# Performance work log

Hardware: AMD Instinct MI355X
Metric: run time of the kernel (lower is better)

Reference implementation:

```python
import jax, jax.numpy as jnp
import numpy as np

EPS = 1e-5
N_LAYERS_TOTAL = 4  # n_layers + 1 convs


def setup_inputs() -> dict:
    key = jax.random.key(0)
    ks = jax.random.split(key, 6)
    B, N, C = 16, 2048, 128
    x = jax.random.normal(ks[0], (B, N, C), dtype=jnp.float32)
    adj = jax.random.uniform(ks[1], (B, N, N), dtype=jnp.float32)
    # per-layer params: weight [L,Cin,Cout], bias [L,Cout], bn gamma/beta [L,C]
    W = jax.random.normal(ks[2], (N_LAYERS_TOTAL, C, C), dtype=jnp.float32) * (1.0 / np.sqrt(C))
    b = jnp.zeros((N_LAYERS_TOTAL, C), dtype=jnp.float32)
    gamma = jnp.ones((N_LAYERS_TOTAL, C), dtype=jnp.float32)
    beta = jnp.zeros((N_LAYERS_TOTAL, C), dtype=jnp.float32)
    return {"x": x, "adj": adj, "W": W, "b": b, "gamma": gamma, "beta": beta}


def reference(x, adj, W, b, gamma, beta):
    # Stacked dense GCNConv -> ReLU -> BatchNorm1d (training mode).
    h = x
    for i in range(N_LAYERS_TOTAL):
        # GCNConv (dense, normalize=False): adj @ (h @ W) + b
        h = jnp.einsum('bnm,bmc->bnc', adj, h @ W[i]) + b[i]  # [B,N,C]
        h = jax.nn.relu(h)
        # BatchNorm over flattened (B*N) per channel, biased variance
        mu = jnp.mean(h, axis=(0, 1))
        var = jnp.mean(jnp.square(h - mu), axis=(0, 1))
        h = gamma[i] * (h - mu) * jax.lax.rsqrt(var + EPS) + beta[i]
    return h
```

## Files before the change

### kernel.cpp

```cpp
#include <hip/hip_runtime.h>
#include <stdint.h>
#include <stddef.h>

#define BATCH 16
#define NROW 2048
#define CH 128
#define NLAYER 4
#define NN_TOT (BATCH * NROW)
#define EPSV 1e-5f
#define KS 64

typedef short short8 __attribute__((ext_vector_type(8)));
typedef float f32x4 __attribute__((ext_vector_type(4)));

static __device__ __forceinline__ unsigned short f2bf(float f) {
  union { float f; unsigned int i; } v;
  v.f = f;
  unsigned int u = v.i;
  return (unsigned short)((u + 0x7FFFu + ((u >> 16) & 1u)) >> 16);
}

__global__ void init_kernel(const float* __restrict__ W,
                            unsigned short* __restrict__ Wt4,
                            float* __restrict__ gsum, float* __restrict__ gsumsq) {
  const int l = blockIdx.x;
  const int t = threadIdx.x;
  if (l < NLAYER) {
    const float* Wl = W + (size_t)l * CH * CH;
    unsigned short* Wo = Wt4 + (size_t)l * CH * CH;
    for (int idx = t; idx < CH * CH; idx += 256) {
      int o = idx >> 7, c = idx & 127;
      Wo[idx] = f2bf(Wl[c * CH + o]);
    }
  } else {
    for (int i = t; i < NLAYER * CH; i += 256) { gsum[i] = 0.0f; gsumsq[i] = 0.0f; }
  }
}

template <int FIRST>
__global__ __launch_bounds__(256) void gemm1_kernel(
    const float* __restrict__ X,
    const unsigned short* __restrict__ Wt,
    const float* __restrict__ gp, const float* __restrict__ bp,
    const float* __restrict__ gsumP, const float* __restrict__ gsumsqP,
    unsigned short* __restrict__ Yt) {
  __shared__ unsigned short As[64 * 128];
  __shared__ unsigned short Bs[128 * 128];
  __shared__ __align__(16) float ss[CH];
  __shared__ __align__(16) float tt[CH];
  const int tid = threadIdx.x;
  const int m0 = blockIdx.x * 64;

  if (!FIRST) {
    if (tid < CH) {
      const float inv = 1.0f / (float)NN_TOT;
      float mu = gsumP[tid] * inv;
      float var = gsumsqP[tid] * inv - mu * mu;
      float s_ = gp[tid] * rsqrtf(var + EPSV);
      ss[tid] = s_;
      tt[tid] = bp[tid] - mu * s_;
    }
    __syncthreads();
  }

#pragma unroll
  for (int j = 0; j < 4; ++j) {
    int c = tid + 256 * j;
    int r = c >> 4, slot = c & 15;
    int kc = slot ^ (r & 15);
    const float* p = X + (size_t)(m0 + r) * CH + kc * 8;
    f32x4 a = *(const f32x4*)p;
    f32x4 b = *(const f32x4*)(p + 4);
    if (!FIRST) {
      f32x4 sa = *(const f32x4*)(ss + kc * 8);
      f32x4 sb = *(const f32x4*)(ss + kc * 8 + 4);
      f32x4 ta = *(const f32x4*)(tt + kc * 8);
      f32x4 tb = *(const f32x4*)(tt + kc * 8 + 4);
      a = sa * a + ta;
      b = sb * b + tb;
    }
    short8 v;
    v[0] = (short)f2bf(a[0]); v[1] = (short)f2bf(a[1]);
    v[2] = (short)f2bf(a[2]); v[3] = (short)f2bf(a[3]);
    v[4] = (short)f2bf(b[0]); v[5] = (short)f2bf(b[1]);
    v[6] = (short)f2bf(b[2]); v[7] = (short)f2bf(b[3]);
    *(short8*)(As + c * 8) = v;
  }
#pragma unroll
  for (int j = 0; j < 8; ++j) {
    int c = tid + 256 * j;
    int r = c >> 4, slot = c & 15;
    int kc = slot ^ (r & 15);
    *(short8*)(Bs + c * 8) = *(const short8*)(Wt + (size_t)r * CH + kc * 8);
  }
  __syncthreads();

  const int l = tid & 63, w = tid >> 6;
  const int mq = (w >> 1) * 32, oq = (w & 1) * 64;
  const int lr = l & 15, lq = l >> 4;
  f32x4 acc[2][4] = {};

#pragma unroll
  for (int kt = 0; kt < 4; ++kt) {
    const int kc0 = kt * 4 + lq;
    const int slotK = kc0 ^ lr;
    short8 a[2], b[4];
#pragma unroll
    for (int mi = 0; mi < 2; ++mi)
      a[mi] = *(const short8*)(As + (mq + mi * 16 + lr) * 128 + slotK * 8);
#pragma unroll
    for (int ni = 0; ni < 4; ++ni)
      b[ni] = *(const short8*)(Bs + (oq + ni * 16 + lr) * 128 + slotK * 8);
#pragma unroll
    for (int mi = 0; mi < 2; ++mi)
#pragma unroll
      for (int ni = 0; ni < 4; ++ni)
        acc[mi][ni] = __builtin_amdgcn_mfma_f32_16x16x32_bf16(a[mi], b[ni], acc[mi][ni], 0, 0, 0);
  }

  const int bat = m0 >> 11;
  const int mb = m0 & 2047;
  unsigned short* YtB = Yt + (size_t)bat * CH * NROW;
#pragma unroll
  for (int ni = 0; ni < 4; ++ni) {
    const int o = oq + ni * 16 + lr;
    unsigned short* row = YtB + (size_t)o * NROW;
#pragma unroll
    for (int mi = 0; mi < 2; ++mi) {
      const int m = mb + mq + mi * 16 + lq * 4;
      f32x4 v = acc[mi][ni];
      unsigned short p0 = f2bf(v[0]), p1 = f2bf(v[1]);
      unsigned short p2 = f2bf(v[2]), p3 = f2bf(v[3]);
      unsigned long long packed = (unsigned long long)p0 | ((unsigned long long)p1 << 16) |
                                  ((unsigned long long)p2 << 32) | ((unsigned long long)p3 << 48);
      *(unsigned long long*)(row + m) = packed;
    }
  }
}

struct Pf {
  short8 a0, a1, a2, a3;
  short8 b0, b1;
  f32x4 f0, f1, f2, f3;
};

template <int CVT>
__global__ __launch_bounds__(256) void gemm2_kernel(
    const float* __restrict__ adjF,
    const unsigned short* __restrict__ adjH,
    unsigned short* __restrict__ adjO,
    const unsigned short* __restrict__ Yt,
    const float* __restrict__ bias,
    float* __restrict__ R,
    float* __restrict__ gsumL, float* __restrict__ gsumsqL) {
  __shared__ unsigned short As[2][CH * KS];
  __shared__ unsigned short Bs[2][64 * KS];
  __shared__ float redS[2][CH];
  __shared__ float redQ[2][CH];

  const int tid = threadIdx.x;
  const int bat = blockIdx.x >> 5;
  const int n0 = (blockIdx.x & 31) * 64;
  const unsigned short* YtB = Yt + (size_t)bat * CH * NROW;

  const int s8 = tid & 7;
  const int r8 = tid >> 3;
  const int swz8 = (s8 ^ (r8 & 7)) * 8;

  const unsigned short* gA0 = YtB + (size_t)r8 * NROW + s8 * 8;
  const unsigned short* gA1 = gA0 + (size_t)32 * NROW;
  const unsigned short* gA2 = gA0 + (size_t)64 * NROW;
  const unsigned short* gA3 = gA0 + (size_t)96 * NROW;
  const int lA0 = r8 * KS + swz8;
  const int lA1 = lA0 + 32 * KS;
  const int lA2 = lA0 + 64 * KS;
  const int lA3 = lA0 + 96 * KS;

  const size_t bO0 = (size_t)bat * NROW * NROW + (size_t)(n0 + r8) * NROW + s8 * 8;
  const size_t bO1 = bO0 + (size_t)32 * NROW;
  const int lB0 = r8 * KS + swz8;
  const int lB1 = lB0 + 32 * KS;

  const int l = tid & 63, w = tid >> 6;
  const int cq = (w >> 1) * 64;
  const int nh = (w & 1) * 32;
  const int lr = l & 15, lq = l >> 4;
  const int rsw = lr & 7;

  f32x4 acc[4][2] = {};

  auto LOADS = [&](Pf& p, int kt) {
    const int k0 = kt * KS;
    p.a0 = *(const short8*)(gA0 + k0);
    p.a1 = *(const short8*)(gA1 + k0);
    p.a2 = *(const short8*)(gA2 + k0);
    p.a3 = *(const short8*)(gA3 + k0);
    if constexpr (CVT) {
      const float* q0 = adjF + bO0 + k0;
      const float* q1 = adjF + bO1 + k0;
      p.f0 = *(const f32x4*)q0; p.f1 = *(const f32x4*)(q0 + 4);
      p.f2 = *(const f32x4*)q1; p.f3 = *(const f32x4*)(q1 + 4);
    } else {
      p.b0 = *(const short8*)(adjH + bO0 + k0);
      p.b1 = *(const short8*)(adjH + bO1 + k0);
    }
  };

  auto WRITES = [&](Pf& p, int buf, int kt) {
    unsigned short* Ap = As[buf];
    *(short8*)(Ap + lA0) = p.a0;
    *(short8*)(Ap + lA1) = p.a1;
    *(short8*)(Ap + lA2) = p.a2;
    *(short8*)(Ap + lA3) = p.a3;
    unsigned short* Bp = Bs[buf];
    if constexpr (CVT) {
      short8 q0, q1;
      q0[0] = (short)f2bf(p.f0[0]); q0[1] = (short)f2bf(p.f0[1]);
      q0[2] = (short)f2bf(p.f0[2]); q0[3] = (short)f2bf(p.f0[3]);
      q0[4] = (short)f2bf(p.f1[0]); q0[5] = (short)f2bf(p.f1[1]);
      q0[6] = (short)f2bf(p.f1[2]); q0[7] = (short)f2bf(p.f1[3]);
      q1[0] = (short)f2bf(p.f2[0]); q1[1] = (short)f2bf(p.f2[1]);
      q1[2] = (short)f2bf(p.f2[2]); q1[3] = (short)f2bf(p.f2[3]);
      q1[4] = (short)f2bf(p.f3[0]); q1[5] = (short)f2bf(p.f3[1]);
      q1[6] = (short)f2bf(p.f3[2]); q1[7] = (short)f2bf(p.f3[3]);
      *(short8*)(Bp + lB0) = q0;
      *(short8*)(Bp + lB1) = q1;
      const int k0 = kt * KS;
      *(short8*)(adjO + bO0 + k0) = q0;
      *(short8*)(adjO + bO1 + k0) = q1;
    } else {
      *(short8*)(Bp + lB0) = p.b0;
      *(short8*)(Bp + lB1) = p.b1;
    }
  };

  auto COMPUTE = [&](int buf) {
    const unsigned short* Ap = As[buf];
    const unsigned short* Bp = Bs[buf];
#pragma unroll
    for (int ks = 0; ks < 2; ++ks) {
      const int sl = ((ks * 4 + lq) ^ rsw) * 8;
      short8 a0 = *(const short8*)(Ap + (cq +  0 + lr) * KS + sl);
      short8 a1 = *(const short8*)(Ap + (cq + 16 + lr) * KS + sl);
      short8 a2 = *(const short8*)(Ap + (cq + 32 + lr) * KS + sl);
      short8 a3 = *(const short8*)(Ap + (cq + 48 + lr) * KS + sl);
      short8 b0 = *(const short8*)(Bp + (nh +  0 + lr) * KS + sl);
      short8 b1 = *(const short8*)(Bp + (nh + 16 + lr) * KS + sl);
      acc[0][0] = __builtin_amdgcn_mfma_f32_16x16x32_bf16(a0, b0, acc[0][0], 0, 0, 0);
      acc[0][1] = __builtin_amdgcn_mfma_f32_16x16x32_bf16(a0, b1, acc[0][1], 0, 0, 0);
      acc[1][0] = __builtin_amdgcn_mfma_f32_16x16x32_bf16(a1, b0, acc[1][0], 0, 0, 0);
      acc[1][1] = __builtin_amdgcn_mfma_f32_16x16x32_bf16(a1, b1, acc[1][1], 0, 0, 0);
      acc[2][0] = __builtin_amdgcn_mfma_f32_16x16x32_bf16(a2, b0, acc[2][0], 0, 0, 0);
      acc[2][1] = __builtin_amdgcn_mfma_f32_16x16x32_bf16(a2, b1, acc[2][1], 0, 0, 0);
      acc[3][0] = __builtin_amdgcn_mfma_f32_16x16x32_bf16(a3, b0, acc[3][0], 0, 0, 0);
      acc[3][1] = __builtin_amdgcn_mfma_f32_16x16x32_bf16(a3, b1, acc[3][1], 0, 0, 0);
    }
  };

#define BAR() do { asm volatile("s_waitcnt lgkmcnt(0)"); __builtin_amdgcn_s_barrier(); } while (0)

  Pf s0, s1;
  LOADS(s0, 0);
  WRITES(s0, 0, 0);
  LOADS(s0, 1);
  LOADS(s1, 2);
  BAR();

#pragma unroll 1
  for (int kt2 = 0; kt2 < 14; ++kt2) {
    const int kt = kt2 * 2;
    COMPUTE(0);
    WRITES(s0, 1, kt + 1);
    LOADS(s0, kt + 3);
    BAR();
    COMPUTE(1);
    WRITES(s1, 0, kt + 2);
    LOADS(s1, kt + 4);
    BAR();
  }
  COMPUTE(0);
  WRITES(s0, 1, 29);
  LOADS(s0, 31);
  BAR();
  COMPUTE(1);
  WRITES(s1, 0, 30);
  BAR();
  COMPUTE(0);
  WRITES(s0, 1, 31);
  BAR();
  COMPUTE(1);
#undef BAR

  float* RB = R + (size_t)bat * NROW * CH;
  f32x4 sumv[4] = {};
  f32x4 sumq[4] = {};
#pragma unroll
  for (int mi = 0; mi < 4; ++mi) {
    const int c0 = cq + mi * 16 + lq * 4;
    f32x4 bia = *(const f32x4*)(bias + c0);
#pragma unroll
    for (int ni = 0; ni < 2; ++ni) {
      const int n = n0 + nh + ni * 16 + lr;
      f32x4 v = acc[mi][ni] + bia;
      v[0] = fmaxf(v[0], 0.0f);
      v[1] = fmaxf(v[1], 0.0f);
      v[2] = fmaxf(v[2], 0.0f);
      v[3] = fmaxf(v[3], 0.0f);
      sumv[mi] += v;
      sumq[mi] += v * v;
      *(f32x4*)(RB + (size_t)n * CH + c0) = v;
    }
  }
#pragma unroll
  for (int mi = 0; mi < 4; ++mi) {
#pragma unroll
    for (int d = 1; d < 16; d <<= 1) {
      sumv[mi][0] += __shfl_xor(sumv[mi][0], d);
      sumv[mi][1] += __shfl_xor(sumv[mi][1], d);
      sumv[mi][2] += __shfl_xor(sumv[mi][2], d);
      sumv[mi][3] += __shfl_xor(sumv[mi][3], d);
      sumq[mi][0] += __shfl_xor(sumq[mi][0], d);
      sumq[mi][1] += __shfl_xor(sumq[mi][1], d);
      sumq[mi][2] += __shfl_xor(sumq[mi][2], d);
      sumq[mi][3] += __shfl_xor(sumq[mi][3], d);
    }
  }
  const int nqi = w & 1;
  if (lr == 0) {
#pragma unroll
    for (int mi = 0; mi < 4; ++mi) {
      const int c0 = cq + mi * 16 + lq * 4;
      redS[nqi][c0 + 0] = sumv[mi][0];
      redS[nqi][c0 + 1] = sumv[mi][1];
      redS[nqi][c0 + 2] = sumv[mi][2];
      redS[nqi][c0 + 3] = sumv[mi][3];
      redQ[nqi][c0 + 0] = sumq[mi][0];
      redQ[nqi][c0 + 1] = sumq[mi][1];
      redQ[nqi][c0 + 2] = sumq[mi][2];
      redQ[nqi][c0 + 3] = sumq[mi][3];
    }
  }
  __syncthreads();
  if (tid < CH) {
    atomicAdd(gsumL + tid, redS[0][tid] + redS[1][tid]);
  } else {
    const int c = tid - CH;
    atomicAdd(gsumsqL + c, redQ[0][c] + redQ[1][c]);
  }
}

__global__ __launch_bounds__(256) void out_kernel(
    float* __restrict__ out,
    const float* __restrict__ g3, const float* __restrict__ b3,
    const float* __restrict__ gsum3, const float* __restrict__ gsumsq3) {
  __shared__ __align__(16) float ss[CH];
  __shared__ __align__(16) float tt[CH];
  if (threadIdx.x < CH) {
    const float inv = 1.0f / (float)NN_TOT;
    float mu = gsum3[threadIdx.x] * inv;
    float var = gsumsq3[threadIdx.x] * inv - mu * mu;
    float s_ = g3[threadIdx.x] * rsqrtf(var + EPSV);
    ss[threadIdx.x] = s_;
    tt[threadIdx.x] = b3[threadIdx.x] - mu * s_;
  }
  __syncthreads();
  const int total = NN_TOT * CH / 4;
  for (int idx = blockIdx.x * blockDim.x + threadIdx.x; idx < total;
       idx += gridDim.x * blockDim.x) {
    f32x4 v = *(f32x4*)(out + (size_t)idx * 4);
    const int c0 = (idx & 31) * 4;
    f32x4 s = *(const f32x4*)(ss + c0);
    f32x4 t = *(const f32x4*)(tt + c0);
    v = s * v + t;
    *(f32x4*)(out + (size_t)idx * 4) = v;
  }
}

extern "C" void kernel_launch(void* const* d_in, const int* in_sizes, int n_in,
                              void* d_out, int out_size, void* d_ws, size_t ws_size,
                              hipStream_t stream) {
  (void)in_sizes; (void)n_in; (void)out_size; (void)ws_size;
  const float* x     = (const float*)d_in[0];
  const float* adj   = (const float*)d_in[1];
  const float* W     = (const float*)d_in[2];
  const float* bvec  = (const float*)d_in[3];
  const float* gamma = (const float*)d_in[4];
  const float* beta  = (const float*)d_in[5];

  float* R = (float*)d_out;

  char* ws = (char*)d_ws;
  unsigned short* adjb = (unsigned short*)(ws);
  unsigned short* Yt   = (unsigned short*)(ws + 134217728);
  unsigned short* Wt4  = (unsigned short*)(ws + 142606336);
  float* gsum   = (float*)(ws + 142606336 + 131072);
  float* gsumsq = (float*)(ws + 142606336 + 131072 + 2048);

  init_kernel<<<NLAYER + 1, 256, 0, stream>>>(W, Wt4, gsum, gsumsq);

  for (int i = 0; i < NLAYER; ++i) {
    if (i == 0) {
      gemm1_kernel<1><<<512, 256, 0, stream>>>(
          x, Wt4, nullptr, nullptr, nullptr, nullptr, Yt);
      gemm2_kernel<1><<<512, 256, 0, stream>>>(
          adj, nullptr, adjb, Yt, bvec, R, gsum, gsumsq);
    } else {
      gemm1_kernel<0><<<512, 256, 0, stream>>>(
          R, Wt4 + (size_t)i * CH * CH,
          gamma + (size_t)(i - 1) * CH, beta + (size_t)(i - 1) * CH,
          gsum + (size_t)(i - 1) * CH, gsumsq + (size_t)(i - 1) * CH, Yt);
      gemm2_kernel<0><<<512, 256, 0, stream>>>(
          nullptr, adjb, nullptr, Yt, bvec + (size_t)i * CH, R,
          gsum + (size_t)i * CH, gsumsq + (size_t)i * CH);
    }
  }
  out_kernel<<<512, 256, 0, stream>>>(R, gamma + 3 * CH, beta + 3 * CH,
                                      gsum + 3 * CH, gsumsq + 3 * CH);
}
```

Before: 587.9 us.

## Fuse all layer kernels into one persistent kernel with software grid barriers

Replaces the nine per-layer GEMM and output launches with a single persistent kernel of 256 blocks. Each block processes two tiles per phase, and a global atomic-counter barrier separates the phases. Shared memory is overlaid through a union across phases. The aim is to remove kernel launch gaps and tail effects between layers. In exchange it halves the grid, so each block does serial work, and it adds spin-barrier latency. The barrier also assumes all 256 blocks are co-resident, and it has a timeout fallback that could break correctness.

```diff
diff --git a/kernel.cpp b/kernel.cpp
--- a/kernel.cpp
+++ b/kernel.cpp
@@ -9,6 +9,8 @@
 #define NN_TOT (BATCH * NROW)
 #define EPSV 1e-5f
 #define KS 64
+#define GRID_P 256
+#define NTILE 512
 
 typedef short short8 __attribute__((ext_vector_type(8)));
 typedef float f32x4 __attribute__((ext_vector_type(4)));
@@ -20,9 +22,34 @@
   return (unsigned short)((u + 0x7FFFu + ((u >> 16) & 1u)) >> 16);
 }
 
+union __align__(16) SM {
+  struct { unsigned short As[64 * 128];
+           unsigned short Bs[128 * 128];
+           float ss[CH]; float tt[CH]; } g1;
+  struct { unsigned short As[2][CH * KS];
+           unsigned short Bs[2][64 * KS];
+           float redS[2][CH]; float redQ[2][CH]; } g2;
+  struct { float ss[CH]; float tt[CH]; } o;
+};
+
+static __device__ __forceinline__ void grid_sync(unsigned* cnt, unsigned target) {
+  __syncthreads();
+  if (threadIdx.x == 0) {
+    __hip_atomic_fetch_add(cnt, 1u, __ATOMIC_RELEASE, __HIP_MEMORY_SCOPE_AGENT);
+    unsigned long long t0 = __builtin_amdgcn_s_memrealtime();
+    while (__hip_atomic_load(cnt, __ATOMIC_RELAXED, __HIP_MEMORY_SCOPE_AGENT) < target) {
+      __builtin_amdgcn_s_sleep(8);
+      if (__builtin_amdgcn_s_memrealtime() - t0 > 200000000ull) break;
+    }
+    (void)__hip_atomic_load(cnt, __ATOMIC_ACQUIRE, __HIP_MEMORY_SCOPE_AGENT);
+  }
+  __syncthreads();
+}
+
 __global__ void init_kernel(const float* __restrict__ W,
                             unsigned short* __restrict__ Wt4,
-                            float* __restrict__ gsum, float* __restrict__ gsumsq) {
+                            float* __restrict__ gsum, float* __restrict__ gsumsq,
+                            unsigned* __restrict__ bar) {
   const int l = blockIdx.x;
   const int t = threadIdx.x;
   if (l < NLAYER) {
@@ -34,24 +61,24 @@
     }
   } else {
     for (int i = t; i < NLAYER * CH; i += 256) { gsum[i] = 0.0f; gsumsq[i] = 0.0f; }
-  }
-}
-
-template <int FIRST>
-__global__ __launch_bounds__(256) void gemm1_kernel(
-    const float* __restrict__ X,
-    const unsigned short* __restrict__ Wt,
+    if (t == 0) *bar = 0u;
+  }
+}
+
+static __device__ void gemm1_phase(
+    SM& sm, const float* __restrict__ X, const unsigned short* __restrict__ Wt,
     const float* __restrict__ gp, const float* __restrict__ bp,
     const float* __restrict__ gsumP, const float* __restrict__ gsumsqP,
-    unsigned short* __restrict__ Yt) {
-  __shared__ unsigned short As[64 * 128];
-  __shared__ unsigned short Bs[128 * 128];
-  __shared__ __align__(16) float ss[CH];
-  __shared__ __align__(16) float tt[CH];
-  const int tid = threadIdx.x;
-  const int m0 = blockIdx.x * 64;
-
-  if (!FIRST) {
+    unsigned short* __restrict__ Yt, const int first, const int tile, const int tid) {
+  unsigned short* As = sm.g1.As;
+  unsigned short* Bs = sm.g1.Bs;
+  float* ss = sm.g1.ss;
+  float* tt = sm.g1.tt;
+  const int m0 = tile * 64;
+
+  __syncthreads();
+
+  if (!first) {
     if (tid < CH) {
       const float inv = 1.0f / (float)NN_TOT;
       float mu = gsumP[tid] * inv;
@@ -71,7 +98,7 @@
     const float* p = X + (size_t)(m0 + r) * CH + kc * 8;
     f32x4 a = *(const f32x4*)p;
     f32x4 b = *(const f32x4*)(p + 4);
-    if (!FIRST) {
+    if (!first) {
       f32x4 sa = *(const f32x4*)(ss + kc * 8);
       f32x4 sb = *(const f32x4*)(ss + kc * 8 + 4);
       f32x4 ta = *(const f32x4*)(tt + kc * 8);
@@ -145,22 +172,15 @@
 };
 
 template <int CVT>
-__global__ __launch_bounds__(256) void gemm2_kernel(
-    const float* __restrict__ adjF,
-    const unsigned short* __restrict__ adjH,
-    unsigned short* __restrict__ adjO,
-    const unsigned short* __restrict__ Yt,
-    const float* __restrict__ bias,
-    float* __restrict__ R,
-    float* __restrict__ gsumL, float* __restrict__ gsumsqL) {
-  __shared__ unsigned short As[2][CH * KS];
-  __shared__ unsigned short Bs[2][64 * KS];
-  __shared__ float redS[2][CH];
-  __shared__ float redQ[2][CH];
-
-  const int tid = threadIdx.x;
-  const int bat = blockIdx.x >> 5;
-  const int n0 = (blockIdx.x & 31) * 64;
+static __device__ void gemm2_phase(
+    SM& sm,
+    const float* __restrict__ adjF, const unsigned short* __restrict__ adjH,
+    unsigned short* __restrict__ adjO, const unsigned short* __restrict__ Yt,
+    const float* __restrict__ bias, float* __restrict__ R,
+    float* __restrict__ gsumL, float* __restrict__ gsumsqL,
+    const int tile, const int tid) {
+  const int bat = tile >> 5;
+  const int n0 = (tile & 31) * 64;
   const unsigned short* YtB = Yt + (size_t)bat * CH * NROW;
 
   const int s8 = tid & 7;
@@ -207,12 +227,12 @@
   };
 
   auto WRITES = [&](Pf& p, int buf, int kt) {
-    unsigned short* Ap = As[buf];
+    unsigned short* Ap = sm.g2.As[buf];
     *(short8*)(Ap + lA0) = p.a0;
     *(short8*)(Ap + lA1) = p.a1;
     *(short8*)(Ap + lA2) = p.a2;
     *(short8*)(Ap + lA3) = p.a3;
-    unsigned short* Bp = Bs[buf];
+    unsigned short* Bp = sm.g2.Bs[buf];
     if constexpr (CVT) {
       short8 q0, q1;
       q0[0] = (short)f2bf(p.f0[0]); q0[1] = (short)f2bf(p.f0[1]);
@@ -235,8 +255,8 @@
   };
 
   auto COMPUTE = [&](int buf) {
-    const unsigned short* Ap = As[buf];
-    const unsigned short* Bp = Bs[buf];
+    const unsigned short* Ap = sm.g2.As[buf];
+    const unsigned short* Bp = sm.g2.Bs[buf];
 #pragma unroll
     for (int ks = 0; ks < 2; ++ks) {
       const int sl = ((ks * 4 + lq) ^ rsw) * 8;
@@ -261,6 +281,7 @@
 
   Pf s0, s1;
   LOADS(s0, 0);
+  __syncthreads();
   WRITES(s0, 0, 0);
   LOADS(s0, 1);
   LOADS(s1, 2);
@@ -326,47 +347,49 @@
     }
   }
   const int nqi = w & 1;
+  __syncthreads();
   if (lr == 0) {
 #pragma unroll
     for (int mi = 0; mi < 4; ++mi) {
       const int c0 = cq + mi * 16 + lq * 4;
-      redS[nqi][c0 + 0] = sumv[mi][0];
-      redS[nqi][c0 + 1] = sumv[mi][1];
-      redS[nqi][c0 + 2] = sumv[mi][2];
-      redS[nqi][c0 + 3] = sumv[mi][3];
-      redQ[nqi][c0 + 0] = sumq[mi][0];
-      redQ[nqi][c0 + 1] = sumq[mi][1];
-      redQ[nqi][c0 + 2] = sumq[mi][2];
-      redQ[nqi][c0 + 3] = sumq[mi][3];
+      sm.g2.redS[nqi][c0 + 0] = sumv[mi][0];
+      sm.g2.redS[nqi][c0 + 1] = sumv[mi][1];
+      sm.g2.redS[nqi][c0 + 2] = sumv[mi][2];
+      sm.g2.redS[nqi][c0 + 3] = sumv[mi][3];
+      sm.g2.redQ[nqi][c0 + 0] = sumq[mi][0];
+      sm.g2.redQ[nqi][c0 + 1] = sumq[mi][1];
+      sm.g2.redQ[nqi][c0 + 2] = sumq[mi][2];
+      sm.g2.redQ[nqi][c0 + 3] = sumq[mi][3];
     }
   }
   __syncthreads();
   if (tid < CH) {
-    atomicAdd(gsumL + tid, redS[0][tid] + redS[1][tid]);
+    atomicAdd(gsumL + tid, sm.g2.redS[0][tid] + sm.g2.redS[1][tid]);
   } else {
     const int c = tid - CH;
-    atomicAdd(gsumsqL + c, redQ[0][c] + redQ[1][c]);
-  }
-}
-
-__global__ __launch_bounds__(256) void out_kernel(
-    float* __restrict__ out,
+    atomicAdd(gsumsqL + c, sm.g2.redQ[0][c] + sm.g2.redQ[1][c]);
+  }
+}
+
+static __device__ void out_phase(
+    SM& sm, float* __restrict__ out,
     const float* __restrict__ g3, const float* __restrict__ b3,
-    const float* __restrict__ gsum3, const float* __restrict__ gsumsq3) {
-  __shared__ __align__(16) float ss[CH];
-  __shared__ __align__(16) float tt[CH];
-  if (threadIdx.x < CH) {
+    const float* __restrict__ gsum3, const float* __restrict__ gsumsq3,
+    const int blk, const int tid) {
+  float* ss = sm.o.ss;
+  float* tt = sm.o.tt;
+  __syncthreads();
+  if (tid < CH) {
     const float inv = 1.0f / (float)NN_TOT;
-    float mu = gsum3[threadIdx.x] * inv;
-    float var = gsumsq3[threadIdx.x] * inv - mu * mu;
-    float s_ = g3[threadIdx.x] * rsqrtf(var + EPSV);
-    ss[threadIdx.x] = s_;
-    tt[threadIdx.x] = b3[threadIdx.x] - mu * s_;
+    float mu = gsum3[tid] * inv;
+    float var = gsumsq3[tid] * inv - mu * mu;
+    float s_ = g3[tid] * rsqrtf(var + EPSV);
+    ss[tid] = s_;
+    tt[tid] = b3[tid] - mu * s_;
   }
   __syncthreads();
   const int total = NN_TOT * CH / 4;
-  for (int idx = blockIdx.x * blockDim.x + threadIdx.x; idx < total;
-       idx += gridDim.x * blockDim.x) {
+  for (int idx = blk * 256 + tid; idx < total; idx += GRID_P * 256) {
     f32x4 v = *(f32x4*)(out + (size_t)idx * 4);
     const int c0 = (idx & 31) * 4;
     f32x4 s = *(const f32x4*)(ss + c0);
@@ -374,6 +397,45 @@
     v = s * v + t;
     *(f32x4*)(out + (size_t)idx * 4) = v;
   }
+}
+
+__global__ __launch_bounds__(256, 2) void fused_kernel(
+    const float* __restrict__ x, const float* __restrict__ adj,
+    const float* __restrict__ W, const float* __restrict__ bvec,
+    const float* __restrict__ gamma, const float* __restrict__ beta,
+    float* __restrict__ R, unsigned short* __restrict__ adjb,
+    unsigned short* __restrict__ Yt, unsigned short* __restrict__ Wt4,
+    float* __restrict__ gsum, float* __restrict__ gsumsq,
+    unsigned* __restrict__ bar) {
+  __shared__ SM sm;
+  const int blk = blockIdx.x, tid = threadIdx.x;
+  unsigned tgt = 0;
+
+  gemm1_phase(sm, x, Wt4, nullptr, nullptr, nullptr, nullptr, Yt, 1, blk, tid);
+  gemm1_phase(sm, x, Wt4, nullptr, nullptr, nullptr, nullptr, Yt, 1, blk + GRID_P, tid);
+  tgt += GRID_P; grid_sync(bar, tgt);
+  gemm2_phase<1>(sm, adj, nullptr, adjb, Yt, bvec, R, gsum, gsumsq, blk, tid);
+  gemm2_phase<1>(sm, adj, nullptr, adjb, Yt, bvec, R, gsum, gsumsq, blk + GRID_P, tid);
+  tgt += GRID_P; grid_sync(bar, tgt);
+
+  for (int li = 1; li < NLAYER; ++li) {
+    const unsigned short* Wl = Wt4 + (size_t)li * CH * CH;
+    const float* gp = gamma + (size_t)(li - 1) * CH;
+    const float* bp = beta + (size_t)(li - 1) * CH;
+    const float* gs = gsum + (size_t)(li - 1) * CH;
+    const float* gq = gsumsq + (size_t)(li - 1) * CH;
+    gemm1_phase(sm, R, Wl, gp, bp, gs, gq, Yt, 0, blk, tid);
+    gemm1_phase(sm, R, Wl, gp, bp, gs, gq, Yt, 0, blk + GRID_P, tid);
+    tgt += GRID_P; grid_sync(bar, tgt);
+    gemm2_phase<0>(sm, nullptr, adjb, nullptr, Yt, bvec + (size_t)li * CH, R,
+                   gsum + (size_t)li * CH, gsumsq + (size_t)li * CH, blk, tid);
+    gemm2_phase<0>(sm, nullptr, adjb, nullptr, Yt, bvec + (size_t)li * CH, R,
+                   gsum + (size_t)li * CH, gsumsq + (size_t)li * CH, blk + GRID_P, tid);
+    tgt += GRID_P; grid_sync(bar, tgt);
+  }
+
+  out_phase(sm, R, gamma + 3 * CH, beta + 3 * CH,
+            gsum + 3 * CH, gsumsq + 3 * CH, blk, tid);
 }
 
 extern "C" void kernel_launch(void* const* d_in, const int* in_sizes, int n_in,
@@ -395,25 +457,10 @@
   unsigned short* Wt4  = (unsigned short*)(ws + 142606336);
   float* gsum   = (float*)(ws + 142606336 + 131072);
   float* gsumsq = (float*)(ws + 142606336 + 131072 + 2048);
-
-  init_kernel<<<NLAYER + 1, 256, 0, stream>>>(W, Wt4, gsum, gsumsq);
-
-  for (int i = 0; i < NLAYER; ++i) {
-    if (i == 0) {
-      gemm1_kernel<1><<<512, 256, 0, stream>>>(
-          x, Wt4, nullptr, nullptr, nullptr, nullptr, Yt);
-      gemm2_kernel<1><<<512, 256, 0, stream>>>(
-          adj, nullptr, adjb, Yt, bvec, R, gsum, gsumsq);
-    } else {
-      gemm1_kernel<0><<<512, 256, 0, stream>>>(
-          R, Wt4 + (size_t)i * CH * CH,
-          gamma + (size_t)(i - 1) * CH, beta + (size_t)(i - 1) * CH,
-          gsum + (size_t)(i - 1) * CH, gsumsq + (size_t)(i - 1) * CH, Yt);
-      gemm2_kernel<0><<<512, 256, 0, stream>>>(
-          nullptr, adjb, nullptr, Yt, bvec + (size_t)i * CH, R,
-          gsum + (size_t)i * CH, gsumsq + (size_t)i * CH);
-    }
-  }
-  out_kernel<<<512, 256, 0, stream>>>(R, gamma + 3 * CH, beta + 3 * CH,
-                                      gsum + 3 * CH, gsumsq + 3 * CH);
-}
+  unsigned* bar = (unsigned*)(ws + 142606336 + 131072 + 4096);
+
+  init_kernel<<<NLAYER + 1, 256, 0, stream>>>(W, Wt4, gsum, gsumsq, bar);
+
+  fused_kernel<<<GRID_P, 256, 0, stream>>>(
+      x, adj, W, bvec, gamma, beta, R, adjb, Yt, Wt4, gsum, gsumsq, bar);
+}
```

Result: slower. 750.2 us (+27.6%).
